# Kernel optimization log

Hardware: AMD Instinct MI355X
Metric: run time of the kernel (lower is better)

The kernel has to match this reference:

```python
import jax, jax.numpy as jnp
import numpy as np
from jax import lax

B, CIN, COUT, K, S, P, H, W = 8, 128, 256, 3, 1, 1, 64, 64


def setup_inputs() -> dict:
    key = jax.random.key(0)
    k1, k2, k3, k4, k5 = jax.random.split(key, 5)
    fan_off = CIN * K * K
    fan_dc = CIN * K * K
    return {
        "x": jax.random.normal(k1, (B, CIN, H, W), dtype=jnp.float32),
        # offset-predicting conv: Conv2d(CIN, 2*K*K, K, S, P, padding_mode='reflect')
        "w_off": jax.random.normal(k2, (2 * K * K, CIN, K, K), dtype=jnp.float32) / np.sqrt(fan_off),
        "b_off": jax.random.normal(k3, (2 * K * K,), dtype=jnp.float32) * 0.01,
        # deformable conv weights: DeformConv2d(CIN, COUT, K, S, P)
        "w_dc": jax.random.normal(k4, (COUT, CIN, K, K), dtype=jnp.float32) / np.sqrt(fan_dc),
        "b_dc": jax.random.normal(k5, (COUT,), dtype=jnp.float32) * 0.01,
    }


def _reflect_conv(x, w, b, stride, pad):
    # Conv2d with reflect padding
    xp = jnp.pad(x, ((0, 0), (0, 0), (pad, pad), (pad, pad)), mode="reflect")
    y = lax.conv_general_dilated(xp, w, (stride, stride), "VALID",
                                 dimension_numbers=("NCHW", "OIHW", "NCHW"))
    return y + b[None, :, None, None]


def _deform_conv(x, offset, w, b, k, stride, pad):
    # torchvision DeformConv2d (v1, no mask, 1 offset group)
    Bn, C, Hi, Wi = x.shape
    Ho, Wo = offset.shape[2], offset.shape[3]
    KK = k * k
    # offset layout: [B, 2*KK, Ho, Wo], interleaved (dy, dx) per kernel position
    off = offset.reshape(Bn, KK, 2, Ho, Wo)
    hb = jnp.arange(Ho, dtype=x.dtype) * stride - pad          # base rows
    wb = jnp.arange(Wo, dtype=x.dtype) * stride - pad          # base cols
    ki, kj = jnp.meshgrid(jnp.arange(k, dtype=x.dtype), jnp.arange(k, dtype=x.dtype), indexing="ij")
    ki, kj = ki.reshape(KK), kj.reshape(KK)
    # sampling locations [B, KK, Ho, Wo]
    py = off[:, :, 0] + hb[None, None, :, None] + ki[None, :, None, None]
    px = off[:, :, 1] + wb[None, None, None, :] + kj[None, :, None, None]
    y0 = jnp.floor(py)
    x0 = jnp.floor(px)
    dy = (py - y0).reshape(Bn, 1, -1)
    dx = (px - x0).reshape(Bn, 1, -1)
    y0i = y0.astype(jnp.int32)
    x0i = x0.astype(jnp.int32)
    xf = x.reshape(Bn, C, Hi * Wi)

    def gather(yi, xi):
        valid = (yi >= 0) & (yi < Hi) & (xi >= 0) & (xi < Wi)
        yc = jnp.clip(yi, 0, Hi - 1)
        xc = jnp.clip(xi, 0, Wi - 1)
        idx = (yc * Wi + xc).reshape(Bn, -1)                   # [B, KK*Ho*Wo]
        g = jax.vmap(lambda xb, ib: xb[:, ib])(xf, idx)        # [B, C, KK*Ho*Wo]
        return g * valid.reshape(Bn, 1, -1).astype(x.dtype)

    v00 = gather(y0i, x0i)
    v01 = gather(y0i, x0i + 1)
    v10 = gather(y0i + 1, x0i)
    v11 = gather(y0i + 1, x0i + 1)
    vals = (v00 * (1 - dy) * (1 - dx) + v01 * (1 - dy) * dx
            + v10 * dy * (1 - dx) + v11 * dy * dx)             # [B, C, KK*Ho*Wo]
    cols = vals.reshape(Bn, C, KK, Ho * Wo)
    out = jnp.einsum("bckl,ock->bol", cols, w.reshape(-1, C, KK))
    out = out + b[None, :, None]
    return out.reshape(Bn, -1, Ho, Wo)


def reference(x, w_off, b_off, w_dc, b_dc):
    x_offset = _reflect_conv(x, w_off, b_off, S, P)            # [B, 2*K*K, Ho, Wo]
    # torch.chunk followed by torch.concat is an identity on the offset tensor
    return _deform_conv(x, x_offset, w_dc, b_dc, K, S, P)
```

## Files before the change

### kernel.cpp

```cpp
#include <hip/hip_runtime.h>
#include <hip/hip_fp16.h>

typedef unsigned short u16;
typedef unsigned int   u32;
typedef u32   u32x2  __attribute__((ext_vector_type(2)));
typedef u32   u32x4  __attribute__((ext_vector_type(4)));
typedef short short8 __attribute__((ext_vector_type(8)));
typedef float f32x4  __attribute__((ext_vector_type(4)));
typedef _Float16 half8 __attribute__((ext_vector_type(8)));

__device__ __forceinline__ u16 f2h(float f) { return __half_as_ushort(__float2half(f)); }
__device__ __forceinline__ f32x4 mfma16(short8 a, short8 b, f32x4 c) {
  return __builtin_amdgcn_mfma_f32_16x16x32_f16(
      __builtin_bit_cast(half8, a), __builtin_bit_cast(half8, b), c, 0, 0, 0);
}
__device__ __forceinline__ __half2 h2cast(u32 u) { return __builtin_bit_cast(__half2, u); }
__device__ __forceinline__ int refl(int v) { return v < 0 ? -v : (v > 63 ? 126 - v : v); }

__device__ __forceinline__ void softbar() {
  asm volatile("s_waitcnt lgkmcnt(0)" ::: "memory");
  __builtin_amdgcn_s_barrier();
  asm volatile("" ::: "memory");
}

__global__ __launch_bounds__(256) void prep_fused(const float* __restrict__ x,
                                                  const float* __restrict__ w_dc,
                                                  const float* __restrict__ w_off,
                                                  u16* __restrict__ xh,
                                                  u16* __restrict__ Wl2,
                                                  u16* __restrict__ Wol2) {
  int bid = blockIdx.x;
  int tid = threadIdx.x;
  if (bid < 512) {
    __shared__ float tile[128][65];
    int swz = (bid & 7) * 64 + (bid >> 3);
    int b = swz >> 6, h = swz & 63;
    for (int i = 0; i < 32; ++i) {
      int c = (tid >> 6) + i * 4;
      int w = tid & 63;
      tile[c][w] = x[(((size_t)b * 128 + c) * 64 + h) * 64 + w];
    }
    __syncthreads();
    u16* dst = xh + ((size_t)(b * 64 + h) * 64) * 128;
    for (int j = 0; j < 32; ++j) {
      int c = tid & 127;
      int w = (tid >> 7) + 2 * j;
      dst[w * 128 + c] = f2h(tile[c][w]);
    }
  } else {
    int idx = (bid - 512) * 256 + tid;
    if (idx < 294912) {
      int e = idx & 7, lane = (idx >> 3) & 63, ks = (idx >> 9) & 3;
      int mt = (idx >> 11) & 15, kk = idx >> 15;
      int o = mt * 16 + (lane & 15), c = ks * 32 + (lane >> 4) * 8 + e;
      Wl2[idx] = f2h(w_dc[(o * 128 + c) * 9 + kk]);
    } else {
      int i2 = idx - 294912;
      int e = i2 & 7, lane = (i2 >> 3) & 63, ks = (i2 >> 9) & 3;
      int mt = (i2 >> 11) & 1, kk = i2 >> 12;
      int co = mt * 16 + (lane & 15), c = ks * 32 + (lane >> 4) * 8 + e;
      Wol2[i2] = (co < 18) ? f2h(w_off[(co * 128 + c) * 9 + kk]) : (u16)0;
    }
  }
}

__device__ __forceinline__ void make_entry_lds(u32x4* __restrict__ tbl, int kk,
                                               int ho, int wo, int lq,
                                               float offy, float offx) {
  int ki = kk / 3, kj = kk - ki * 3;
  float py = offy + (float)(ho + ki - 1);
  float px = offx + (float)(wo + kj - 1);
  float fy0 = floorf(py), fx0 = floorf(px);
  int y0 = (int)fy0, x0 = (int)fx0;
  float fy = py - fy0, fx = px - fx0;
  float w11 = fy * fx, w10 = fy - w11, w01 = fx - w11, w00 = 1.f - fy - fx + w11;
  bool iy0 = (y0 >= 0) & (y0 < 64), iy1 = (y0 >= -1) & (y0 < 63);
  bool ix0 = (x0 >= 0) & (x0 < 64), ix1 = (x0 >= -1) & (x0 < 63);
  int y0c = min(max(y0, 0), 63), x0c = min(max(x0, 0), 63);
  u32 addr00 = (u32)((y0c * 64 + x0c) * 128);
  u32 dx = (x0 >= 0 && x0 < 63) ? 128u : 0u;
  u32 dy = (y0 >= 0 && y0 < 63) ? 8192u : 0u;
  u32 wA = (u32)f2h((iy0 && ix0) ? w00 : 0.f) | ((u32)f2h((iy0 && ix1) ? w01 : 0.f) << 16);
  u32 wB = (u32)f2h((iy1 && ix0) ? w10 : 0.f) | ((u32)f2h((iy1 && ix1) ? w11 : 0.f) << 16);
  u32x4 ent; ent.x = addr00; ent.y = dx | (dy << 16); ent.z = wA; ent.w = wB;
  tbl[kk * 128 + lq] = ent;
}

__global__ __launch_bounds__(1024, 4) void deform_fused(
    const u16* __restrict__ xh, const u16* __restrict__ Wl2,
    const u16* __restrict__ Wol2, const float* __restrict__ b_off,
    const float* __restrict__ b_dc, float* __restrict__ out) {
  __shared__ union SCU {
    u16 slab[4][64][128];
    u16 cols[2][128][128];
  } sc;
  __shared__ u32x4 tbl[9 * 128];

  int bid = blockIdx.x;
  int b = bid & 7, t = bid >> 3;
  int ho0 = t * 2;
  int tid = threadIdx.x, lane = tid & 63, wv = tid >> 6;
  int ln15 = lane & 15, kg = lane >> 4;
  const u16* xb = xh + (size_t)b * 524288;

  {
    u32x4 st[4];
#pragma unroll
    for (int i = 0; i < 4; ++i) {
      int T = tid + i * 1024;
      int r = T >> 10, w = (T >> 4) & 63, cb = (T & 15) * 8;
      int hr = refl(ho0 - 1 + r);
      st[i] = *(const u32x4*)(xb + (hr * 64 + w) * 128 + cb);
    }
#pragma unroll
    for (int i = 0; i < 4; ++i) {
      int T = tid + i * 1024;
      int r = T >> 10, w = (T >> 4) & 63, cb = (T & 15) * 8;
      *(u32x4*)&sc.slab[r][w][cb ^ ((w & 7) << 3)] = st[i];
    }
  }
  __syncthreads();

  int mtA = wv & 1;
  int lq = (wv >> 1) * 16 + ln15;
  int lh = lq >> 6, lw = lq & 63;
  f32x4 oacc = {0.f, 0.f, 0.f, 0.f};
  __builtin_amdgcn_s_setprio(1);
#pragma unroll
  for (int kk = 0; kk < 9; ++kk) {
    int ki = kk / 3, kj = kk - ki * 3;
    int j = refl(lw + kj - 1);
    int row = lh + ki;
    const u16* wb = Wol2 + ((kk * 2 + mtA) * 4) * 512 + lane * 8;
    int sbj = (j & 7) << 3;
#pragma unroll
    for (int ks = 0; ks < 4; ++ks) {
      short8 af = *(const short8*)(wb + ks * 512);
      short8 bf = *(const short8*)&sc.slab[row][j][(ks * 32 + kg * 8) ^ sbj];
      oacc = mfma16(af, bf, oacc);
    }
  }
  __builtin_amdgcn_s_setprio(0);

  if (mtA == 0) {
    int kkA = 2 * kg, kkB = 2 * kg + 1;
    make_entry_lds(tbl, kkA, ho0 + lh, lw, lq, oacc[0] + b_off[2 * kkA], oacc[1] + b_off[2 * kkA + 1]);
    make_entry_lds(tbl, kkB, ho0 + lh, lw, lq, oacc[2] + b_off[2 * kkB], oacc[3] + b_off[2 * kkB + 1]);
  } else if (kg == 0) {
    make_entry_lds(tbl, 8, ho0 + lh, lw, lq, oacc[0] + b_off[16], oacc[1] + b_off[17]);
  }
  __syncthreads();

  if (wv >= 8) {
    int pt = tid & 511;
    int tl = pt >> 4;
    int tcl = (pt & 15) * 8;
    int swzc = tcl ^ ((tl & 7) << 3);

    u32x4 gv[4][4];
    u32 gwA[4], gwB[4];
    auto gissue = [&](int g) {
#pragma unroll
      for (int i = 0; i < 4; ++i) {
        int l = tl + i * 32;
        u32x4 e = tbl[g * 128 + l];
        gwA[i] = e.z; gwB[i] = e.w;
        const u16* p = xb + e.x + tcl;
        u32 dxv = e.y & 0xffffu, dyv = e.y >> 16;
        gv[i][0] = *(const u32x4*)p;
        gv[i][1] = *(const u32x4*)(p + dxv);
        gv[i][2] = *(const u32x4*)(p + dyv);
        gv[i][3] = *(const u32x4*)(p + dyv + dxv);
      }
    };
    auto gwrite = [&](int dbuf) {
#pragma unroll
      for (int i = 0; i < 4; ++i) {
        int l = tl + i * 32;
        __half2 wA = h2cast(gwA[i]), wB = h2cast(gwB[i]);
        __half2 w00 = __half2half2(wA.x), w01 = __half2half2(wA.y);
        __half2 w10 = __half2half2(wB.x), w11 = __half2half2(wB.y);
        u32x4 pv;
#pragma unroll
        for (int wd = 0; wd < 4; ++wd) {
          __half2 r = __hmul2(h2cast(gv[i][0][wd]), w00);
          r = __hfma2(h2cast(gv[i][1][wd]), w01, r);
          r = __hfma2(h2cast(gv[i][2][wd]), w10, r);
          r = __hfma2(h2cast(gv[i][3][wd]), w11, r);
          pv[wd] = __builtin_bit_cast(u32, r);
        }
        *(u32x4*)&sc.cols[dbuf][l][swzc] = pv;
      }
    };

    gissue(0); gwrite(0);
    gissue(1);
    softbar();
    for (int kk = 0; kk < 9; ++kk) {
      int cur = kk & 1;
      if (kk < 8) gwrite(cur ^ 1);
      if (kk < 7) gissue(kk + 2);
      softbar();
    }
  } else {
    int cg = wv & 3, lhc = wv >> 2;
    f32x4 acc[4][4];
#pragma unroll
    for (int m = 0; m < 4; ++m)
#pragma unroll
      for (int n = 0; n < 4; ++n) acc[m][n] = (f32x4){0.f, 0.f, 0.f, 0.f};

    int swzb = (ln15 & 7) << 3;
    softbar();
    for (int kk = 0; kk < 9; ++kk) {
      int cur = kk & 1;
      const u16* wb = Wl2 + (size_t)kk * 32768 + lane * 8;
      short8 ac[4], an[4];
#pragma unroll
      for (int m = 0; m < 4; ++m)
        ac[m] = *(const short8*)(wb + (size_t)((cg * 4 + m) * 4) * 512);
#pragma unroll
      for (int ks = 0; ks < 4; ++ks) {
        if (ks < 3) {
#pragma unroll
          for (int m = 0; m < 4; ++m)
            an[m] = *(const short8*)(wb + (size_t)((cg * 4 + m) * 4 + ks + 1) * 512);
        }
        __builtin_amdgcn_s_setprio(1);
#pragma unroll
        for (int nt = 0; nt < 4; ++nt) {
          int l = lhc * 64 + nt * 16 + ln15;
          short8 bf = *(const short8*)&sc.cols[cur][l][(ks * 32 + kg * 8) ^ swzb];
#pragma unroll
          for (int m = 0; m < 4; ++m)
            acc[m][nt] = mfma16(ac[m], bf, acc[m][nt]);
        }
        __builtin_amdgcn_s_setprio(0);
        if (ks < 3) {
#pragma unroll
          for (int m = 0; m < 4; ++m) ac[m] = an[m];
        }
      }
      softbar();
    }

#pragma unroll
    for (int m = 0; m < 4; ++m) {
#pragma unroll
      for (int r = 0; r < 4; ++r) {
        int o = cg * 64 + m * 16 + kg * 4 + r;
        float bias = b_dc[o];
        size_t base = ((size_t)(b * 256 + o)) * 4096 + ho0 * 64 + lhc * 64;
#pragma unroll
        for (int nt = 0; nt < 4; ++nt) {
          out[base + nt * 16 + ln15] = acc[m][nt][r] + bias;
        }
      }
    }
  }
}

extern "C" void kernel_launch(void* const* d_in, const int* in_sizes, int n_in,
                              void* d_out, int out_size, void* d_ws, size_t ws_size,
                              hipStream_t stream) {
  const float* x     = (const float*)d_in[0];
  const float* w_off = (const float*)d_in[1];
  const float* b_off = (const float*)d_in[2];
  const float* w_dc  = (const float*)d_in[3];
  const float* b_dc  = (const float*)d_in[4];
  float* out = (float*)d_out;
  char* ws = (char*)d_ws;
  u16* xh   = (u16*)ws;
  u16* Wl2  = (u16*)(ws + 8388608);
  u16* Wol2 = (u16*)(ws + 8388608 + 589824);
  prep_fused  <<<dim3(1808), dim3(256), 0, stream>>>(x, w_dc, w_off, xh, Wl2, Wol2);
  deform_fused<<<dim3(256),  dim3(1024), 0, stream>>>(xh, Wl2, Wol2, b_off, b_dc, out);
}
```

Baseline: 47.06 us.

## Stage offset-conv and deform-conv weights through LDS instead of global loads

The offset-conv weights are copied into shared memory once per block, and the MFMA waves read them from there. For the main deformable GEMM, the producer waves now prefetch each kernel tap's weight slice into a shared LDS buffer, and a second barrier per tap guards that buffer. The aim is to stop every consumer wave from reloading the same A fragments from global/L2. In exchange, LDS use rises to about 157KB per block, which likely allows only one block per CU, and each loop iteration gains an extra barrier.

```diff
diff --git a/kernel.cpp b/kernel.cpp
--- a/kernel.cpp
+++ b/kernel.cpp
@@ -86,15 +86,15 @@
   tbl[kk * 128 + lq] = ent;
 }
 
+struct SMA { u16 slab[4][64][128]; u16 wol[36864]; };
+struct SMB { u16 cols[2][128][128]; u16 abuf[32768]; };
+
 __global__ __launch_bounds__(1024, 4) void deform_fused(
     const u16* __restrict__ xh, const u16* __restrict__ Wl2,
     const u16* __restrict__ Wol2, const float* __restrict__ b_off,
     const float* __restrict__ b_dc, float* __restrict__ out) {
-  __shared__ union SCU {
-    u16 slab[4][64][128];
-    u16 cols[2][128][128];
-  } sc;
-  __shared__ u32x4 tbl[9 * 128];
+  __shared__ union { SMA a; SMB b; } sm;
+  __shared__ u32x4 tbl[1152];
 
   int bid = blockIdx.x;
   int b = bid & 7, t = bid >> 3;
@@ -112,11 +112,22 @@
       int hr = refl(ho0 - 1 + r);
       st[i] = *(const u32x4*)(xb + (hr * 64 + w) * 128 + cb);
     }
+    u32x4 wl[5];
+#pragma unroll
+    for (int i = 0; i < 5; ++i) {
+      int T = tid + i * 1024;
+      if (T < 4608) wl[i] = *(const u32x4*)(Wol2 + T * 8);
+    }
 #pragma unroll
     for (int i = 0; i < 4; ++i) {
       int T = tid + i * 1024;
       int r = T >> 10, w = (T >> 4) & 63, cb = (T & 15) * 8;
-      *(u32x4*)&sc.slab[r][w][cb ^ ((w & 7) << 3)] = st[i];
+      *(u32x4*)&sm.a.slab[r][w][cb ^ ((w & 7) << 3)] = st[i];
+    }
+#pragma unroll
+    for (int i = 0; i < 5; ++i) {
+      int T = tid + i * 1024;
+      if (T < 4608) *(u32x4*)&sm.a.wol[T * 8] = wl[i];
     }
   }
   __syncthreads();
@@ -131,12 +142,12 @@
     int ki = kk / 3, kj = kk - ki * 3;
     int j = refl(lw + kj - 1);
     int row = lh + ki;
-    const u16* wb = Wol2 + ((kk * 2 + mtA) * 4) * 512 + lane * 8;
     int sbj = (j & 7) << 3;
+    int wbase = ((kk * 2 + mtA) * 4) * 512 + lane * 8;
 #pragma unroll
     for (int ks = 0; ks < 4; ++ks) {
-      short8 af = *(const short8*)(wb + ks * 512);
-      short8 bf = *(const short8*)&sc.slab[row][j][(ks * 32 + kg * 8) ^ sbj];
+      short8 af = *(const short8*)&sm.a.wol[wbase + ks * 512];
+      short8 bf = *(const short8*)&sm.a.slab[row][j][(ks * 32 + kg * 8) ^ sbj];
       oacc = mfma16(af, bf, oacc);
     }
   }
@@ -189,17 +200,35 @@
           r = __hfma2(h2cast(gv[i][3][wd]), w11, r);
           pv[wd] = __builtin_bit_cast(u32, r);
         }
-        *(u32x4*)&sc.cols[dbuf][l][swzc] = pv;
-      }
-    };
-
-    gissue(0); gwrite(0);
+        *(u32x4*)&sm.b.cols[dbuf][l][swzc] = pv;
+      }
+    };
+
+    u32x4 sa[8];
+    auto stage_issue = [&](int kk) {
+#pragma unroll
+      for (int j = 0; j < 8; ++j)
+        sa[j] = *(const u32x4*)(Wl2 + (size_t)kk * 32768 + (pt + j * 512) * 8);
+    };
+    auto stage_write = [&]() {
+#pragma unroll
+      for (int j = 0; j < 8; ++j)
+        *(u32x4*)&sm.b.abuf[(pt + j * 512) * 8] = sa[j];
+    };
+
+    stage_issue(0);
+    gissue(0);
+    gwrite(0);
+    stage_write();
     gissue(1);
     softbar();
     for (int kk = 0; kk < 9; ++kk) {
       int cur = kk & 1;
+      if (kk < 8) stage_issue(kk + 1);
       if (kk < 8) gwrite(cur ^ 1);
       if (kk < 7) gissue(kk + 2);
+      softbar();
+      if (kk < 8) stage_write();
       softbar();
     }
   } else {
@@ -214,33 +243,24 @@
     softbar();
     for (int kk = 0; kk < 9; ++kk) {
       int cur = kk & 1;
-      const u16* wb = Wl2 + (size_t)kk * 32768 + lane * 8;
-      short8 ac[4], an[4];
-#pragma unroll
-      for (int m = 0; m < 4; ++m)
-        ac[m] = *(const short8*)(wb + (size_t)((cg * 4 + m) * 4) * 512);
+      __builtin_amdgcn_s_setprio(1);
 #pragma unroll
       for (int ks = 0; ks < 4; ++ks) {
-        if (ks < 3) {
-#pragma unroll
-          for (int m = 0; m < 4; ++m)
-            an[m] = *(const short8*)(wb + (size_t)((cg * 4 + m) * 4 + ks + 1) * 512);
-        }
-        __builtin_amdgcn_s_setprio(1);
+        short8 a[4];
+#pragma unroll
+        for (int m = 0; m < 4; ++m)
+          a[m] = *(const short8*)&sm.b.abuf[((cg * 4 + m) * 4 + ks) * 512 + lane * 8];
 #pragma unroll
         for (int nt = 0; nt < 4; ++nt) {
           int l = lhc * 64 + nt * 16 + ln15;
-          short8 bf = *(const short8*)&sc.cols[cur][l][(ks * 32 + kg * 8) ^ swzb];
+          short8 bf = *(const short8*)&sm.b.cols[cur][l][(ks * 32 + kg * 8) ^ swzb];
 #pragma unroll
           for (int m = 0; m < 4; ++m)
-            acc[m][nt] = mfma16(ac[m], bf, acc[m][nt]);
+            acc[m][nt] = mfma16(a[m], bf, acc[m][nt]);
         }
-        __builtin_amdgcn_s_setprio(0);
-        if (ks < 3) {
-#pragma unroll
-          for (int m = 0; m < 4; ++m) ac[m] = an[m];
-        }
-      }
+      }
+      __builtin_amdgcn_s_setprio(0);
+      softbar();
       softbar();
     }
 
```

Result: slower. 57.09 us (+21.3%).
